# Kernel tuning notes

Hardware: AMD Instinct MI355X
Metric: run time of the kernel (lower is better)

Reference implementation:

```python
import jax, jax.numpy as jnp
import numpy as np


def setup_inputs() -> dict:
    key = jax.random.key(0)
    B, T = 4096, 2048
    # small positive strains keep C = 2E + I symmetric positive definite
    strain = jax.random.uniform(key, (B, T, 3), dtype=jnp.float32) * 0.2
    ki0 = jnp.float32(1.5)  # learned exponent for order-0 stretch term
    ki1 = jnp.float32(1.0)  # scale on log(J) term (init 1.0 in torch code)
    return {"strain": strain, "ki0": ki0, "ki1": ki1}


def reference(strain, ki0, ki1):
    # Build symmetric 2x2 right Cauchy-Green tensor C = 2E + I implicitly:
    # E00 = s0, E11 = s1, E01 = E10 = 0.5*s2  ->  C01 = s2
    c00 = 2.0 * strain[..., 0] + 1.0          # [B, T]
    c11 = 2.0 * strain[..., 1] + 1.0
    c01 = strain[..., 2]

    det = c00 * c11 - c01 * c01               # det(C)
    J = jnp.sqrt(det)
    log_J = jnp.log(J)

    # closed-form eigenvalues of symmetric 2x2, ascending (matches eigvalsh)
    mean = 0.5 * (c00 + c11)
    rad = jnp.sqrt(0.25 * (c00 - c11) ** 2 + c01 * c01)
    sq_eig = jnp.stack([mean - rad, mean + rad], axis=-1)  # [B, T, 2]

    eig = jnp.sqrt(sq_eig)                    # principal stretches
    aux = J ** (-1.0 / 3.0)                   # volumetric regularizer
    reg_eig = eig * aux[..., None]            # [B, T, 2]

    # order_stretches = 1: one powered-stretch block + scaled log(J)
    kan_input = jnp.concatenate(
        [reg_eig ** ki0, (log_J * ki1)[..., None]], axis=-1
    )                                         # [B, T, 3]
    return kan_input
```

## Files before the change

### kernel.cpp

```cpp
#include <hip/hip_runtime.h>


__device__ __forceinline__ void compute3(float s0, float s1, float s2,
                                         float ki0, float ki1,
                                         float& o0, float& o1, float& o2) {
    const float c00 = __builtin_fmaf(2.0f, s0, 1.0f);
    const float c11 = __builtin_fmaf(2.0f, s1, 1.0f);
    const float c01 = s2;
    const float det = c00 * c11 - c01 * c01;
    const float l2det = __builtin_log2f(det);
    const float mean = 0.5f * (c00 + c11);
    const float diff = 0.5f * (c00 - c11);
    const float rad  = __builtin_sqrtf(__builtin_fmaf(diff, diff, c01 * c01));
    const float l2a = -0.16666666667f * l2det;
    o0 = __builtin_exp2f(ki0 * __builtin_fmaf(0.5f, __builtin_log2f(mean - rad), l2a));
    o1 = __builtin_exp2f(ki0 * __builtin_fmaf(0.5f, __builtin_log2f(mean + rad), l2a));
    o2 = (0.34657359028f * l2det) * ki1;
}

__global__ __launch_bounds__(256) void kan_v5_allfp32(
    const float* __restrict__ strain,
    const float* __restrict__ ki0p,
    const float* __restrict__ ki1p,
    float* __restrict__ out,
    long long ntrip)
{
    const float ki0 = ki0p[0];
    const float ki1 = ki1p[0];

    const long long nvec = ntrip >> 3;
    const long long stride = (long long)gridDim.x * 256LL;

    for (long long v = (long long)blockIdx.x * 256LL + threadIdx.x; v < nvec; v += stride) {
        const float4* ip = (const float4*)(strain + v * 24);
        const float4 f0 = ip[0], f1 = ip[1], f2 = ip[2];
        const float4 f3 = ip[3], f4 = ip[4], f5 = ip[5];

        float o[24];
        compute3(f0.x, f0.y, f0.z, ki0, ki1, o[0],  o[1],  o[2]);
        compute3(f0.w, f1.x, f1.y, ki0, ki1, o[3],  o[4],  o[5]);
        compute3(f1.z, f1.w, f2.x, ki0, ki1, o[6],  o[7],  o[8]);
        compute3(f2.y, f2.z, f2.w, ki0, ki1, o[9],  o[10], o[11]);
        compute3(f3.x, f3.y, f3.z, ki0, ki1, o[12], o[13], o[14]);
        compute3(f3.w, f4.x, f4.y, ki0, ki1, o[15], o[16], o[17]);
        compute3(f4.z, f4.w, f5.x, ki0, ki1, o[18], o[19], o[20]);
        compute3(f5.y, f5.z, f5.w, ki0, ki1, o[21], o[22], o[23]);

        float4* op = (float4*)(out + v * 24);
        op[0] = make_float4(o[0],  o[1],  o[2],  o[3]);
        op[1] = make_float4(o[4],  o[5],  o[6],  o[7]);
        op[2] = make_float4(o[8],  o[9],  o[10], o[11]);
        op[3] = make_float4(o[12], o[13], o[14], o[15]);
        op[4] = make_float4(o[16], o[17], o[18], o[19]);
        op[5] = make_float4(o[20], o[21], o[22], o[23]);
    }

    const long long tail_start = nvec << 3;
    for (long long e = tail_start + (long long)blockIdx.x * 256LL + threadIdx.x;
         e < ntrip; e += stride) {
        float o0, o1, o2;
        compute3(strain[3 * e], strain[3 * e + 1], strain[3 * e + 2],
                 ki0, ki1, o0, o1, o2);
        out[3 * e]     = o0;
        out[3 * e + 1] = o1;
        out[3 * e + 2] = o2;
    }
}

extern "C" void kernel_launch(void* const* d_in, const int* in_sizes, int n_in,
                              void* d_out, int out_size, void* d_ws, size_t ws_size,
                              hipStream_t stream) {
    const float* strain = (const float*)d_in[0];
    const float* ki0p   = (const float*)d_in[1];
    const float* ki1p   = (const float*)d_in[2];
    float* out = (float*)d_out;

    const long long ntrip = (long long)in_sizes[0] / 3;
    const long long nvec  = ntrip >> 3;
    long long want_blocks = (nvec + 255) / 256;
    if (want_blocks < 1) want_blocks = 1;
    if (want_blocks > 65535) want_blocks = 65535;

    kan_v5_allfp32<<<(int)want_blocks, 256, 0, stream>>>(strain, ki0p, ki1p, out, ntrip);
}
```

Baseline: 189.0 us.

## Stage input and output tiles through LDS for coalesced float4 global access

Each block now loads a 2048-triplet tile into shared memory with fully coalesced float4 loads, padding rows to seven slots to reduce bank conflicts. Each thread then reads its 24 contiguous floats from LDS, computes, writes the results back to LDS, and the block stores them coalesced. Previously every thread read and wrote six float4 spaced 96 bytes apart, which is uncoalesced across the wavefront. The cost is four block barriers per tile, extra LDS traffic, and a cap of 32768 blocks that turns the kernel into a grid-stride loop.

```diff
diff --git a/kernel.cpp b/kernel.cpp
--- a/kernel.cpp
+++ b/kernel.cpp
@@ -1,5 +1,7 @@
 #include <hip/hip_runtime.h>
 
+
+typedef unsigned int u32;
 
 __device__ __forceinline__ void compute3(float s0, float s1, float s2,
                                          float ki0, float ki1,
@@ -18,46 +20,73 @@
     o2 = (0.34657359028f * l2det) * ki1;
 }
 
-__global__ __launch_bounds__(256) void kan_v5_allfp32(
+constexpr int TPB       = 256;
+constexpr int TRIPT     = 8;
+constexpr int TILE_TRIP = TPB * TRIPT;
+constexpr int CHT       = 6;
+constexpr int TILE_CH   = TPB * CHT;
+constexpr int ROW_SLOTS = 7;
+
+__global__ __launch_bounds__(TPB) void kan_v6_lds(
     const float* __restrict__ strain,
     const float* __restrict__ ki0p,
     const float* __restrict__ ki1p,
     float* __restrict__ out,
     long long ntrip)
 {
+    __shared__ float4 lds4[TPB * ROW_SLOTS];
+
     const float ki0 = ki0p[0];
     const float ki1 = ki1p[0];
+    const int t = threadIdx.x;
+    const long long full_tiles = ntrip / TILE_TRIP;
 
-    const long long nvec = ntrip >> 3;
-    const long long stride = (long long)gridDim.x * 256LL;
+    for (long long tile = blockIdx.x; tile < full_tiles; tile += gridDim.x) {
+        const long long cbase = tile * TILE_CH;
+        const float4* in4 = (const float4*)strain + cbase;
+        float4*      out4 = (float4*)out + cbase;
 
-    for (long long v = (long long)blockIdx.x * 256LL + threadIdx.x; v < nvec; v += stride) {
-        const float4* ip = (const float4*)(strain + v * 24);
-        const float4 f0 = ip[0], f1 = ip[1], f2 = ip[2];
-        const float4 f3 = ip[3], f4 = ip[4], f5 = ip[5];
+        __syncthreads();
+#pragma unroll
+        for (int j = 0; j < CHT; ++j) {
+            const u32 k = (u32)t + (u32)(j * TPB);
+            lds4[(k / 6u) * ROW_SLOTS + (k % 6u)] = in4[k];
+        }
+        __syncthreads();
+
+        const int rb = t * ROW_SLOTS;
+        const float4 r0 = lds4[rb + 0], r1 = lds4[rb + 1], r2 = lds4[rb + 2];
+        const float4 r3 = lds4[rb + 3], r4 = lds4[rb + 4], r5 = lds4[rb + 5];
 
         float o[24];
-        compute3(f0.x, f0.y, f0.z, ki0, ki1, o[0],  o[1],  o[2]);
-        compute3(f0.w, f1.x, f1.y, ki0, ki1, o[3],  o[4],  o[5]);
-        compute3(f1.z, f1.w, f2.x, ki0, ki1, o[6],  o[7],  o[8]);
-        compute3(f2.y, f2.z, f2.w, ki0, ki1, o[9],  o[10], o[11]);
-        compute3(f3.x, f3.y, f3.z, ki0, ki1, o[12], o[13], o[14]);
-        compute3(f3.w, f4.x, f4.y, ki0, ki1, o[15], o[16], o[17]);
-        compute3(f4.z, f4.w, f5.x, ki0, ki1, o[18], o[19], o[20]);
-        compute3(f5.y, f5.z, f5.w, ki0, ki1, o[21], o[22], o[23]);
+        compute3(r0.x, r0.y, r0.z, ki0, ki1, o[0],  o[1],  o[2]);
+        compute3(r0.w, r1.x, r1.y, ki0, ki1, o[3],  o[4],  o[5]);
+        compute3(r1.z, r1.w, r2.x, ki0, ki1, o[6],  o[7],  o[8]);
+        compute3(r2.y, r2.z, r2.w, ki0, ki1, o[9],  o[10], o[11]);
+        compute3(r3.x, r3.y, r3.z, ki0, ki1, o[12], o[13], o[14]);
+        compute3(r3.w, r4.x, r4.y, ki0, ki1, o[15], o[16], o[17]);
+        compute3(r4.z, r4.w, r5.x, ki0, ki1, o[18], o[19], o[20]);
+        compute3(r5.y, r5.z, r5.w, ki0, ki1, o[21], o[22], o[23]);
 
-        float4* op = (float4*)(out + v * 24);
-        op[0] = make_float4(o[0],  o[1],  o[2],  o[3]);
-        op[1] = make_float4(o[4],  o[5],  o[6],  o[7]);
-        op[2] = make_float4(o[8],  o[9],  o[10], o[11]);
-        op[3] = make_float4(o[12], o[13], o[14], o[15]);
-        op[4] = make_float4(o[16], o[17], o[18], o[19]);
-        op[5] = make_float4(o[20], o[21], o[22], o[23]);
+        __syncthreads();
+        lds4[rb + 0] = make_float4(o[0],  o[1],  o[2],  o[3]);
+        lds4[rb + 1] = make_float4(o[4],  o[5],  o[6],  o[7]);
+        lds4[rb + 2] = make_float4(o[8],  o[9],  o[10], o[11]);
+        lds4[rb + 3] = make_float4(o[12], o[13], o[14], o[15]);
+        lds4[rb + 4] = make_float4(o[16], o[17], o[18], o[19]);
+        lds4[rb + 5] = make_float4(o[20], o[21], o[22], o[23]);
+        __syncthreads();
+
+#pragma unroll
+        for (int j = 0; j < CHT; ++j) {
+            const u32 k = (u32)t + (u32)(j * TPB);
+            out4[k] = lds4[(k / 6u) * ROW_SLOTS + (k % 6u)];
+        }
     }
 
-    const long long tail_start = nvec << 3;
-    for (long long e = tail_start + (long long)blockIdx.x * 256LL + threadIdx.x;
-         e < ntrip; e += stride) {
+    const long long tail_start = full_tiles * TILE_TRIP;
+    const long long gs = (long long)gridDim.x * TPB;
+    for (long long e = tail_start + (long long)blockIdx.x * TPB + t; e < ntrip; e += gs) {
         float o0, o1, o2;
         compute3(strain[3 * e], strain[3 * e + 1], strain[3 * e + 2],
                  ki0, ki1, o0, o1, o2);
@@ -76,10 +105,9 @@
     float* out = (float*)d_out;
 
     const long long ntrip = (long long)in_sizes[0] / 3;
-    const long long nvec  = ntrip >> 3;
-    long long want_blocks = (nvec + 255) / 256;
-    if (want_blocks < 1) want_blocks = 1;
-    if (want_blocks > 65535) want_blocks = 65535;
+    long long blocks = ntrip / TILE_TRIP;
+    if (blocks < 1) blocks = 1;
+    if (blocks > 32768) blocks = 32768;
 
-    kan_v5_allfp32<<<(int)want_blocks, 256, 0, stream>>>(strain, ki0p, ki1p, out, ntrip);
+    kan_v6_lds<<<(int)blocks, TPB, 0, stream>>>(strain, ki0p, ki1p, out, ntrip);
 }
```

New measurement: 180.5 us. 1.05x faster.
